# Kernel optimization log

Measured on AMD Instinct MI355X. Metric: run time of the kernel, lower is better.

The kernel has to match this reference:

```python
import jax, jax.numpy as jnp
import numpy as np

HIDDEN = 768
PDIM = int(HIDDEN / 4.67)  # 164
QK_DIM = 16
EPS = 1e-5


def setup_inputs() -> dict:
    key = jax.random.key(0)
    k_hs, k_qkv, k_out = jax.random.split(key, 3)
    B, S = 8, 2048
    hidden_states = jax.random.normal(k_hs, (B, S, HIDDEN), dtype=jnp.float32)
    qkv_out = 2 * QK_DIM + PDIM  # 196
    qkv_w = jax.random.normal(k_qkv, (qkv_out, PDIM), dtype=jnp.float32) * (PDIM ** -0.5)
    qkv_b = jnp.zeros((qkv_out,), dtype=jnp.float32)
    out_w = jax.random.normal(k_out, (HIDDEN, HIDDEN), dtype=jnp.float32) * (HIDDEN ** -0.5)
    out_b = jnp.zeros((HIDDEN,), dtype=jnp.float32)
    ln_scale = jnp.ones((PDIM,), dtype=jnp.float32)
    ln_bias = jnp.zeros((PDIM,), dtype=jnp.float32)
    return {
        "hidden_states": hidden_states,
        "ln_scale": ln_scale,
        "ln_bias": ln_bias,
        "qkv_w": qkv_w,
        "qkv_b": qkv_b,
        "out_w": out_w,
        "out_b": out_b,
    }


def reference(hidden_states, ln_scale, ln_bias, qkv_w, qkv_b, out_w, out_b):
    # channel split
    x1 = hidden_states[..., :PDIM]   # [B,S,pdim]
    x2 = hidden_states[..., PDIM:]   # [B,S,hidden-pdim]
    # LayerNorm over last dim
    mean = jnp.mean(x1, axis=-1, keepdims=True)
    var = jnp.mean(jnp.square(x1 - mean), axis=-1, keepdims=True)
    x1n = (x1 - mean) * jax.lax.rsqrt(var + EPS) * ln_scale + ln_bias
    # qkv projection: [B,S,2*qk+pdim]
    qkv = jnp.einsum("bsd,od->bso", x1n, qkv_w) + qkv_b
    q = qkv[..., :QK_DIM]
    k = qkv[..., QK_DIM:2 * QK_DIM]
    v = qkv[..., 2 * QK_DIM:]
    scale = QK_DIM ** -0.5
    scores = jnp.einsum("bqd,bkd->bqk", q, k) * scale  # [B,S,S]
    probs = jax.nn.softmax(scores, axis=-1)
    attended = jnp.einsum("bqk,bkd->bqd", probs, v)  # [B,S,pdim]
    merged = jnp.concatenate([attended, x2], axis=-1)  # [B,S,hidden]
    out = jnp.einsum("bsd,od->bso", merged, out_w) + out_b
    return out
```

## Files before the change

kernel.cpp:

```cpp
#include <hip/hip_runtime.h>
#include <hip/hip_bf16.h>

#define HID 768
#define PD 164
#define NQ 196
#define SEQ 2048

typedef __attribute__((ext_vector_type(8))) short bf16x8_t;
typedef __attribute__((ext_vector_type(4))) float f32x4_t;
typedef __attribute__((ext_vector_type(16))) float f32x16_t;
typedef __attribute__((ext_vector_type(4))) unsigned int u32x4_t;

static __device__ __forceinline__ unsigned short f2bfu(float f) {
  union { __hip_bfloat16 h; unsigned short u; } cv;
  cv.h = __float2bfloat16(f);
  return cv.u;
}

static __device__ __forceinline__ unsigned cvtpk(float a, float b) {
  unsigned r;
  asm("v_cvt_pk_bf16_f32 %0, %1, %2" : "=v"(r) : "v"(a), "v"(b));
  return r;
}

static __device__ __forceinline__ void gload16(const void* g, void* l) {
  __builtin_amdgcn_global_load_lds(
      (const __attribute__((address_space(1))) void*)g,
      (__attribute__((address_space(3))) void*)l, 16, 0, 0);
}

__global__ __launch_bounds__(256) void k_prep_q(const float* __restrict__ qkv_w,
                                                unsigned short* __restrict__ qwb) {
  int i = (blockIdx.x * 256 + threadIdx.x) * 4;
  if (i >= 39936) return;
  int n = i / 192, k = i - n * 192;
  float v0 = (n < NQ && k + 0 < PD) ? qkv_w[n * PD + k + 0] : 0.f;
  float v1 = (n < NQ && k + 1 < PD) ? qkv_w[n * PD + k + 1] : 0.f;
  float v2 = (n < NQ && k + 2 < PD) ? qkv_w[n * PD + k + 2] : 0.f;
  float v3 = (n < NQ && k + 3 < PD) ? qkv_w[n * PD + k + 3] : 0.f;
  ushort4 o;
  o.x = f2bfu(v0); o.y = f2bfu(v1); o.z = f2bfu(v2); o.w = f2bfu(v3);
  *(ushort4*)(qwb + i) = o;
}

__global__ __launch_bounds__(256, 2) void k_lnqkv(const float* __restrict__ hidden,
                                                  const float* __restrict__ lns,
                                                  const float* __restrict__ lnb,
                                                  const unsigned short* __restrict__ qwb,
                                                  const float* __restrict__ qkv_b,
                                                  const float* __restrict__ out_w,
                                                  unsigned short* __restrict__ wbo,
                                                  unsigned short* __restrict__ merged,
                                                  unsigned short* __restrict__ qg,
                                                  unsigned short* __restrict__ kg,
                                                  unsigned short* __restrict__ v16) {
  __shared__ float xr[64][172];
  __shared__ float stats[64][2];
  __shared__ unsigned short Aq[64][200];
  int t = threadIdx.x;
  if (blockIdx.x >= 256) {
    int i = ((blockIdx.x - 256) * 256 + t) * 4;
    float4 v = *(const float4*)(out_w + i);
    ushort4 o;
    o.x = f2bfu(v.x); o.y = f2bfu(v.y); o.z = f2bfu(v.z); o.w = f2bfu(v.w);
    *(ushort4*)(wbo + i) = o;
    return;
  }
  int r0 = blockIdx.x * 64;
  #pragma unroll
  for (int i = 0; i < 11; i++) {
    int idx = t + i * 256;
    if (idx < 2624) {
      int row = idx / 41, q = idx - row * 41;
      float4 v = *(const float4*)(hidden + (size_t)(r0 + row) * HID + q * 4);
      *(float4*)&xr[row][q * 4] = v;
    }
  }
  __syncthreads();
  {
    int l = t & 63, w = t >> 6;
    int row = w * 16 + (l & 15), g = l >> 4;
    float sum = 0.f, sq = 0.f;
    #pragma unroll
    for (int j = 0; j < 41; j++) {
      float x = xr[row][g * 41 + j];
      sum += x; sq += x * x;
    }
    sum += __shfl_xor(sum, 16, 64); sum += __shfl_xor(sum, 32, 64);
    sq  += __shfl_xor(sq, 16, 64);  sq  += __shfl_xor(sq, 32, 64);
    float mean = sum * (1.f / PD);
    float var = sq * (1.f / PD) - mean * mean;
    float rstd = rsqrtf(var + 1e-5f);
    if (g == 0) { stats[row][0] = mean; stats[row][1] = rstd; }
  }
  __syncthreads();
  #pragma unroll
  for (int i = 0; i < 24; i++) {
    int idx = t + i * 256;
    int row = idx / 96, c2 = idx - row * 96;
    int d = c2 * 2;
    float mean = stats[row][0], rstd = stats[row][1];
    float v0 = (d < PD)     ? (xr[row][d]     - mean) * rstd * lns[d]     + lnb[d]     : 0.f;
    float v1 = (d + 1 < PD) ? (xr[row][d + 1] - mean) * rstd * lns[d + 1] + lnb[d + 1] : 0.f;
    unsigned int pk = (unsigned int)f2bfu(v0) | ((unsigned int)f2bfu(v1) << 16);
    *(unsigned int*)(&Aq[row][d]) = pk;
  }
  #pragma unroll
  for (int i = 0; i < 38; i++) {
    int idx = t + i * 256;
    if (idx < 9664) {
      int row = idx / 151, q = idx - row * 151;
      int d = PD + q * 4;
      float4 v = *(const float4*)(hidden + (size_t)(r0 + row) * HID + d);
      ushort4 o;
      o.x = f2bfu(v.x); o.y = f2bfu(v.y); o.z = f2bfu(v.z); o.w = f2bfu(v.w);
      *(ushort4*)(merged + (size_t)(r0 + row) * HID + d) = o;
    }
  }
  __syncthreads();
  int l = t & 63, w = t >> 6, lr15 = l & 15, g = l >> 4;
  f32x4_t acc[13];
  #pragma unroll
  for (int n = 0; n < 13; n++) acc[n] = (f32x4_t){0.f, 0.f, 0.f, 0.f};
  #pragma unroll 2
  for (int kc = 0; kc < 6; kc++) {
    bf16x8_t a = *(const bf16x8_t*)(&Aq[w * 16 + lr15][kc * 32 + g * 8]);
    #pragma unroll
    for (int n = 0; n < 13; n++) {
      bf16x8_t b = *(const bf16x8_t*)(qwb + (size_t)(n * 16 + lr15) * 192 + kc * 32 + g * 8);
      acc[n] = __builtin_amdgcn_mfma_f32_16x16x32_bf16(a, b, acc[n], 0, 0, 0);
    }
  }
  {
    float bias = qkv_b[lr15];
    #pragma unroll
    for (int r = 0; r < 4; r++) {
      int grow = r0 + w * 16 + g * 4 + r;
      qg[(size_t)grow * 16 + lr15] = f2bfu((acc[0][r] + bias) * 0.36067376022224085f);
    }
  }
  {
    float bias = qkv_b[16 + lr15];
    #pragma unroll
    for (int r = 0; r < 4; r++) {
      int grow = r0 + w * 16 + g * 4 + r;
      kg[(size_t)grow * 16 + lr15] = f2bfu(acc[1][r] + bias);
    }
  }
  int s0 = (r0 & 2047) + w * 16;
  int bb = r0 >> 11;
  size_t vrowbase = (size_t)(bb * 128 + (s0 >> 4)) * 192;
  #pragma unroll
  for (int n = 2; n < 13; n++) {
    int col = n * 16 + lr15;
    int d = col - 32;
    float bias = (col < NQ) ? qkv_b[col] : 0.f;
    float v0 = acc[n][0] + bias, v1 = acc[n][1] + bias;
    float v2 = acc[n][2] + bias, v3 = acc[n][3] + bias;
    if (d == 164) { v0 = v1 = v2 = v3 = 1.f; }
    else if (d >= PD) { v0 = v1 = v2 = v3 = 0.f; }
    ushort4 o;
    o.x = f2bfu(v0); o.y = f2bfu(v1); o.z = f2bfu(v2); o.w = f2bfu(v3);
    *(ushort4*)(v16 + (vrowbase + d) * 16 + g * 4) = o;
  }
}

__global__ __launch_bounds__(256, 2) void k_attn(const unsigned short* __restrict__ qg,
                                                 const unsigned short* __restrict__ kg,
                                                 const unsigned short* __restrict__ v16,
                                                 unsigned short* __restrict__ merged) {
  __shared__ float red[2][64 * 98];
  int t = threadIdx.x;
  int w = t >> 6, l = t & 63;
  int b = blockIdx.x & 7, qt = blockIdx.x >> 3;
  int lo = l & 31, hi = l >> 5;
  int qbase = b * SEQ + qt * 32;
  bf16x8_t qf = *(const bf16x8_t*)(qg + (size_t)(qbase + lo) * 16 + hi * 8);
  const unsigned short* kb = kg + (size_t)b * SEQ * 16;
  const unsigned short* vbb = v16 + (size_t)b * 128 * 192 * 16;
  f32x16_t zro;
  #pragma unroll
  for (int r = 0; r < 16; r++) zro[r] = 0.f;
  f32x16_t acc[6];
  #pragma unroll
  for (int f = 0; f < 6; f++) acc[f] = zro;

  int it0 = w * 8;
  bf16x8_t kf0 = *(const bf16x8_t*)(kb + (size_t)(it0 * 64 + lo) * 16 + hi * 8);
  bf16x8_t kf1 = *(const bf16x8_t*)(kb + (size_t)(it0 * 64 + 32 + lo) * 16 + hi * 8);
  bf16x8_t va[6], vb_[6];
  {
    const unsigned short* vt0 = vbb + (size_t)(it0 * 4) * (192 * 16) + hi * 8;
    #pragma unroll
    for (int f = 0; f < 6; f++) va[f] = *(const bf16x8_t*)(vt0 + (f * 32 + lo) * 16);
  }
  for (int it = it0; it < it0 + 8; ++it) {
    bf16x8_t nk0 = *(const bf16x8_t*)(kb + (size_t)((it + 1) * 64 + lo) * 16 + hi * 8);
    bf16x8_t nk1 = *(const bf16x8_t*)(kb + (size_t)((it + 1) * 64 + 32 + lo) * 16 + hi * 8);
    f32x16_t sc0 = __builtin_amdgcn_mfma_f32_32x32x16_bf16(kf0, qf, zro, 0, 0, 0);
    f32x16_t sc1 = __builtin_amdgcn_mfma_f32_32x32x16_bf16(kf1, qf, zro, 0, 0, 0);
    bf16x8_t pa[4];
    #pragma unroll
    for (int jt = 0; jt < 2; ++jt) {
      f32x16_t sc = jt ? sc1 : sc0;
      unsigned u[8];
      #pragma unroll
      for (int k = 0; k < 8; ++k)
        u[k] = cvtpk(exp2f(sc[2 * k]), exp2f(sc[2 * k + 1]));
      asm volatile("v_permlane32_swap_b32 %0, %1" : "+v"(u[0]), "+v"(u[2]));
      asm volatile("v_permlane32_swap_b32 %0, %1" : "+v"(u[1]), "+v"(u[3]));
      asm volatile("v_permlane32_swap_b32 %0, %1" : "+v"(u[4]), "+v"(u[6]));
      asm volatile("v_permlane32_swap_b32 %0, %1" : "+v"(u[5]), "+v"(u[7]));
      union { u32x4_t u4; bf16x8_t h8; } c0, c1;
      c0.u4 = (u32x4_t){u[0], u[1], u[2], u[3]};
      c1.u4 = (u32x4_t){u[4], u[5], u[6], u[7]};
      pa[jt * 2 + 0] = c0.h8;
      pa[jt * 2 + 1] = c1.h8;
    }
#define PV_STEP(JS, VCUR, VNXT, NT, NJS)                                            \
    {                                                                               \
      const unsigned short* vtn = vbb + (size_t)((NT) * 4 + (NJS)) * (192 * 16) + hi * 8; \
      _Pragma("unroll")                                                             \
      for (int f = 0; f < 6; f++) VNXT[f] = *(const bf16x8_t*)(vtn + (f * 32 + lo) * 16); \
      _Pragma("unroll")                                                             \
      for (int f = 0; f < 6; f++)                                                   \
        acc[f] = __builtin_amdgcn_mfma_f32_32x32x16_bf16(pa[JS], VCUR[f], acc[f], 0, 0, 0); \
    }
    PV_STEP(0, va,  vb_, it, 1)
    PV_STEP(1, vb_, va,  it, 2)
    PV_STEP(2, va,  vb_, it, 3)
    PV_STEP(3, vb_, va,  it + 1, 0)
#undef PV_STEP
    kf0 = nk0; kf1 = nk1;
  }

  if (w >= 2) {
    float* dst = &red[w - 2][l * 98];
    #pragma unroll
    for (int f = 0; f < 6; f++)
      #pragma unroll
      for (int r = 0; r < 16; r += 2)
        *(float2*)(dst + f * 16 + r) = make_float2(acc[f][r], acc[f][r + 1]);
  }
  __syncthreads();
  if (w < 2) {
    const float* src = &red[w][l * 98];
    #pragma unroll
    for (int f = 0; f < 6; f++)
      #pragma unroll
      for (int r = 0; r < 16; r += 2) {
        float2 v = *(const float2*)(src + f * 16 + r);
        acc[f][r] += v.x; acc[f][r + 1] += v.y;
      }
  }
  __syncthreads();
  if (w == 1) {
    float* dst = &red[0][l * 98];
    #pragma unroll
    for (int f = 0; f < 6; f++)
      #pragma unroll
      for (int r = 0; r < 16; r += 2)
        *(float2*)(dst + f * 16 + r) = make_float2(acc[f][r], acc[f][r + 1]);
  }
  __syncthreads();
  if (w == 0) {
    const float* src = &red[0][l * 98];
    #pragma unroll
    for (int f = 0; f < 6; f++)
      #pragma unroll
      for (int r = 0; r < 16; r += 2) {
        float2 v = *(const float2*)(src + f * 16 + r);
        acc[f][r] += v.x; acc[f][r + 1] += v.y;
      }
    float dninv[16];
    #pragma unroll
    for (int r = 0; r < 16; ++r)
      dninv[r] = 1.0f / __shfl(acc[5][r], 4 + hi * 32, 64);
    #pragma unroll
    for (int f = 0; f < 6; ++f) {
      int d = f * 32 + lo;
      if (d < PD) {
        #pragma unroll
        for (int r = 0; r < 16; ++r) {
          int q = qbase + (r & 3) + 8 * (r >> 2) + 4 * hi;
          merged[(size_t)q * HID + d] = f2bfu(acc[f][r] * dninv[r]);
        }
      }
    }
  }
}

__global__ __launch_bounds__(256, 3) void k_out(const unsigned short* __restrict__ mg,
                                                const unsigned short* __restrict__ wb,
                                                const float* __restrict__ out_b,
                                                float* __restrict__ out) {
  __shared__ unsigned short Al[2][128 * 32];
  __shared__ unsigned short Bl[2][128 * 32];
  int t = threadIdx.x;
  int bid = blockIdx.x;
  int wgid = (bid & 7) * 96 + (bid >> 3);
  int nb = wgid % 6, mb = wgid / 6;
  int m0 = mb * 128, n0 = nb * 128;
  int l = t & 63, w = t >> 6, wr = w >> 1, wc = w & 1;
  int lr = l & 15, lg = l >> 4;
  int sw = (lr >> 1) & 3;
  f32x4_t acc[4][4];
  #pragma unroll
  for (int mi = 0; mi < 4; mi++)
    #pragma unroll
    for (int ni = 0; ni < 4; ni++) acc[mi][ni] = (f32x4_t){0.f, 0.f, 0.f, 0.f};

  auto stage = [&](int buf, int kt) {
    #pragma unroll
    for (int i = 0; i < 2; i++) {
      int off = t + i * 256;
      int row = off >> 2, c = off & 3;
      int cs = c ^ ((row >> 1) & 3);
      gload16(mg + (size_t)(m0 + row) * HID + kt * 32 + cs * 8, (char*)&Al[buf][0] + off * 16);
    }
    #pragma unroll
    for (int i = 0; i < 2; i++) {
      int off = t + i * 256;
      int row = off >> 2, c = off & 3;
      int cs = c ^ ((row >> 1) & 3);
      gload16(wb + (size_t)(n0 + row) * HID + kt * 32 + cs * 8, (char*)&Bl[buf][0] + off * 16);
    }
  };
  auto compute = [&](int cur) {
    __builtin_amdgcn_s_setprio(1);
    bf16x8_t a[4], bfr[4];
    int slot = lg ^ sw;
    #pragma unroll
    for (int mi = 0; mi < 4; mi++)
      a[mi] = *(const bf16x8_t*)(&Al[cur][(wr * 64 + mi * 16 + lr) * 32 + slot * 8]);
    #pragma unroll
    for (int ni = 0; ni < 4; ni++)
      bfr[ni] = *(const bf16x8_t*)(&Bl[cur][(wc * 64 + ni * 16 + lr) * 32 + slot * 8]);
    #pragma unroll
    for (int mi = 0; mi < 4; mi++)
      #pragma unroll
      for (int ni = 0; ni < 4; ni++)
        acc[mi][ni] = __builtin_amdgcn_mfma_f32_16x16x32_bf16(a[mi], bfr[ni], acc[mi][ni], 0, 0, 0);
    __builtin_amdgcn_s_setprio(0);
  };

  stage(0, 0);
  stage(1, 1);
  for (int kt = 0; kt < 23; kt++) {
    int cur = kt & 1;
    asm volatile("s_waitcnt vmcnt(4)" ::: "memory");
    __builtin_amdgcn_sched_barrier(0);
    __builtin_amdgcn_s_barrier();
    compute(cur);
    asm volatile("s_waitcnt lgkmcnt(0)" ::: "memory");
    __builtin_amdgcn_sched_barrier(0);
    __builtin_amdgcn_s_barrier();
    if (kt + 2 < 24) stage(cur, kt + 2);
  }
  asm volatile("s_waitcnt vmcnt(0)" ::: "memory");
  __builtin_amdgcn_sched_barrier(0);
  __builtin_amdgcn_s_barrier();
  compute(1);

  #pragma unroll
  for (int ni = 0; ni < 4; ni++) {
    int col = n0 + wc * 64 + ni * 16 + lr;
    float bias = out_b[col];
    #pragma unroll
    for (int mi = 0; mi < 4; mi++) {
      #pragma unroll
      for (int r = 0; r < 4; r++) {
        int row = m0 + wr * 64 + mi * 16 + lg * 4 + r;
        out[(size_t)row * HID + col] = acc[mi][ni][r] + bias;
      }
    }
  }
}

extern "C" void kernel_launch(void* const* d_in, const int* in_sizes, int n_in,
                              void* d_out, int out_size, void* d_ws, size_t ws_size,
                              hipStream_t stream) {
  const float* hidden = (const float*)d_in[0];
  const float* lns    = (const float*)d_in[1];
  const float* lnb    = (const float*)d_in[2];
  const float* qkv_w  = (const float*)d_in[3];
  const float* qkv_b  = (const float*)d_in[4];
  const float* out_w  = (const float*)d_in[5];
  const float* out_b  = (const float*)d_in[6];
  char* ws = (char*)d_ws;
  unsigned short* qg  = (unsigned short*)(ws + 0);
  unsigned short* kg  = (unsigned short*)(ws + 524288);
  unsigned short* v16 = (unsigned short*)(ws + 1048576);
  unsigned short* qwb = (unsigned short*)(ws + 13631488);
  unsigned short* wb  = (unsigned short*)(ws + 13711360);
  unsigned short* mg  = (unsigned short*)(ws + 14891008);
  hipLaunchKernelGGL(k_prep_q, dim3(39),  dim3(256), 0, stream, qkv_w, qwb);
  hipLaunchKernelGGL(k_lnqkv,  dim3(832), dim3(256), 0, stream, hidden, lns, lnb, qwb, qkv_b,
                     out_w, wb, mg, qg, kg, v16);
  hipLaunchKernelGGL(k_attn,   dim3(512), dim3(256), 0, stream, qg, kg, v16, mg);
  hipLaunchKernelGGL(k_out,    dim3(768), dim3(256), 0, stream, mg, wb, out_b, (float*)d_out);
}
```

Before: 96.77 us.

## Halve LN+QKV row tile to 32 and split N columns across waves

The LayerNorm+QKV kernel now processes 32 rows per block instead of 64, doubling the grid to 512 compute blocks plus the weight-conversion blocks, and raises the occupancy hint to 4 blocks per CU. Within the QKV MFMA stage, the four waves split as two row groups times two column halves (7 and 6 N-tiles), cutting accumulator registers per wave. The LN statistics loop is vectorised with float4 loads and an 8-lane reduction. The aim is more parallelism and occupancy for this memory-bound prologue, at the cost of reloading qwb B fragments across more blocks.

Result: faster. 93.80 us (-3.1%).

```diff
diff --git a/kernel.cpp b/kernel.cpp
--- a/kernel.cpp
+++ b/kernel.cpp
@@ -43,7 +43,7 @@
   *(ushort4*)(qwb + i) = o;
 }
 
-__global__ __launch_bounds__(256, 2) void k_lnqkv(const float* __restrict__ hidden,
+__global__ __launch_bounds__(256, 4) void k_lnqkv(const float* __restrict__ hidden,
                                                   const float* __restrict__ lns,
                                                   const float* __restrict__ lnb,
                                                   const unsigned short* __restrict__ qwb,
@@ -54,23 +54,24 @@
                                                   unsigned short* __restrict__ qg,
                                                   unsigned short* __restrict__ kg,
                                                   unsigned short* __restrict__ v16) {
-  __shared__ float xr[64][172];
-  __shared__ float stats[64][2];
-  __shared__ unsigned short Aq[64][200];
+  __shared__ float xr[32][172];
+  __shared__ float stats[32][2];
+  __shared__ unsigned short Aq[32][200];
   int t = threadIdx.x;
-  if (blockIdx.x >= 256) {
-    int i = ((blockIdx.x - 256) * 256 + t) * 4;
+  if (blockIdx.x >= 512) {
+    int i = ((blockIdx.x - 512) * 256 + t) * 4;
     float4 v = *(const float4*)(out_w + i);
     ushort4 o;
     o.x = f2bfu(v.x); o.y = f2bfu(v.y); o.z = f2bfu(v.z); o.w = f2bfu(v.w);
     *(ushort4*)(wbo + i) = o;
     return;
   }
-  int r0 = blockIdx.x * 64;
-  #pragma unroll
-  for (int i = 0; i < 11; i++) {
+  int r0 = blockIdx.x * 32;
+  int l = t & 63, w = t >> 6;
+  #pragma unroll
+  for (int i = 0; i < 6; i++) {
     int idx = t + i * 256;
-    if (idx < 2624) {
+    if (idx < 1312) {
       int row = idx / 41, q = idx - row * 41;
       float4 v = *(const float4*)(hidden + (size_t)(r0 + row) * HID + q * 4);
       *(float4*)&xr[row][q * 4] = v;
@@ -78,24 +79,23 @@
   }
   __syncthreads();
   {
-    int l = t & 63, w = t >> 6;
-    int row = w * 16 + (l & 15), g = l >> 4;
+    int row = w * 8 + (l & 7), g8 = l >> 3;
     float sum = 0.f, sq = 0.f;
-    #pragma unroll
-    for (int j = 0; j < 41; j++) {
-      float x = xr[row][g * 41 + j];
-      sum += x; sq += x * x;
-    }
-    sum += __shfl_xor(sum, 16, 64); sum += __shfl_xor(sum, 32, 64);
-    sq  += __shfl_xor(sq, 16, 64);  sq  += __shfl_xor(sq, 32, 64);
+    for (int j = g8; j < 41; j += 8) {
+      float4 v = *(const float4*)&xr[row][j * 4];
+      sum += v.x + v.y + v.z + v.w;
+      sq  += v.x * v.x + v.y * v.y + v.z * v.z + v.w * v.w;
+    }
+    sum += __shfl_xor(sum, 8, 64); sum += __shfl_xor(sum, 16, 64); sum += __shfl_xor(sum, 32, 64);
+    sq  += __shfl_xor(sq, 8, 64);  sq  += __shfl_xor(sq, 16, 64);  sq  += __shfl_xor(sq, 32, 64);
     float mean = sum * (1.f / PD);
     float var = sq * (1.f / PD) - mean * mean;
     float rstd = rsqrtf(var + 1e-5f);
-    if (g == 0) { stats[row][0] = mean; stats[row][1] = rstd; }
-  }
-  __syncthreads();
-  #pragma unroll
-  for (int i = 0; i < 24; i++) {
+    if (g8 == 0) { stats[row][0] = mean; stats[row][1] = rstd; }
+  }
+  __syncthreads();
+  #pragma unroll
+  for (int i = 0; i < 12; i++) {
     int idx = t + i * 256;
     int row = idx / 96, c2 = idx - row * 96;
     int d = c2 * 2;
@@ -106,9 +106,9 @@
     *(unsigned int*)(&Aq[row][d]) = pk;
   }
   #pragma unroll
-  for (int i = 0; i < 38; i++) {
+  for (int i = 0; i < 19; i++) {
     int idx = t + i * 256;
-    if (idx < 9664) {
+    if (idx < 4832) {
       int row = idx / 151, q = idx - row * 151;
       int d = PD + q * 4;
       float4 v = *(const float4*)(hidden + (size_t)(r0 + row) * HID + d);
@@ -118,50 +118,69 @@
     }
   }
   __syncthreads();
-  int l = t & 63, w = t >> 6, lr15 = l & 15, g = l >> 4;
-  f32x4_t acc[13];
-  #pragma unroll
-  for (int n = 0; n < 13; n++) acc[n] = (f32x4_t){0.f, 0.f, 0.f, 0.f};
+  int lr15 = l & 15, g = l >> 4;
+  int wr = w & 1, nh = w >> 1;
+  int nbase = nh ? 7 : 0;
+  int ncnt  = nh ? 6 : 7;
+  f32x4_t acc[7];
+  #pragma unroll
+  for (int n = 0; n < 7; n++) acc[n] = (f32x4_t){0.f, 0.f, 0.f, 0.f};
   #pragma unroll 2
   for (int kc = 0; kc < 6; kc++) {
-    bf16x8_t a = *(const bf16x8_t*)(&Aq[w * 16 + lr15][kc * 32 + g * 8]);
-    #pragma unroll
-    for (int n = 0; n < 13; n++) {
-      bf16x8_t b = *(const bf16x8_t*)(qwb + (size_t)(n * 16 + lr15) * 192 + kc * 32 + g * 8);
-      acc[n] = __builtin_amdgcn_mfma_f32_16x16x32_bf16(a, b, acc[n], 0, 0, 0);
-    }
-  }
-  {
-    float bias = qkv_b[lr15];
-    #pragma unroll
-    for (int r = 0; r < 4; r++) {
-      int grow = r0 + w * 16 + g * 4 + r;
-      qg[(size_t)grow * 16 + lr15] = f2bfu((acc[0][r] + bias) * 0.36067376022224085f);
-    }
-  }
-  {
-    float bias = qkv_b[16 + lr15];
-    #pragma unroll
-    for (int r = 0; r < 4; r++) {
-      int grow = r0 + w * 16 + g * 4 + r;
-      kg[(size_t)grow * 16 + lr15] = f2bfu(acc[1][r] + bias);
-    }
-  }
-  int s0 = (r0 & 2047) + w * 16;
+    bf16x8_t a = *(const bf16x8_t*)(&Aq[wr * 16 + lr15][kc * 32 + g * 8]);
+    #pragma unroll
+    for (int ni = 0; ni < 7; ni++) {
+      if (ni < ncnt) {
+        int n = nbase + ni;
+        bf16x8_t b = *(const bf16x8_t*)(qwb + (size_t)(n * 16 + lr15) * 192 + kc * 32 + g * 8);
+        acc[ni] = __builtin_amdgcn_mfma_f32_16x16x32_bf16(a, b, acc[ni], 0, 0, 0);
+      }
+    }
+  }
+  int s0 = (r0 & 2047) + wr * 16;
   int bb = r0 >> 11;
   size_t vrowbase = (size_t)(bb * 128 + (s0 >> 4)) * 192;
-  #pragma unroll
-  for (int n = 2; n < 13; n++) {
-    int col = n * 16 + lr15;
-    int d = col - 32;
-    float bias = (col < NQ) ? qkv_b[col] : 0.f;
-    float v0 = acc[n][0] + bias, v1 = acc[n][1] + bias;
-    float v2 = acc[n][2] + bias, v3 = acc[n][3] + bias;
-    if (d == 164) { v0 = v1 = v2 = v3 = 1.f; }
-    else if (d >= PD) { v0 = v1 = v2 = v3 = 0.f; }
-    ushort4 o;
-    o.x = f2bfu(v0); o.y = f2bfu(v1); o.z = f2bfu(v2); o.w = f2bfu(v3);
-    *(ushort4*)(v16 + (vrowbase + d) * 16 + g * 4) = o;
+  if (nh == 0) {
+    {
+      float bias = qkv_b[lr15];
+      #pragma unroll
+      for (int r = 0; r < 4; r++) {
+        int grow = r0 + wr * 16 + g * 4 + r;
+        qg[(size_t)grow * 16 + lr15] = f2bfu((acc[0][r] + bias) * 0.36067376022224085f);
+      }
+    }
+    {
+      float bias = qkv_b[16 + lr15];
+      #pragma unroll
+      for (int r = 0; r < 4; r++) {
+        int grow = r0 + wr * 16 + g * 4 + r;
+        kg[(size_t)grow * 16 + lr15] = f2bfu(acc[1][r] + bias);
+      }
+    }
+    #pragma unroll
+    for (int ni = 2; ni < 7; ni++) {
+      int col = ni * 16 + lr15;
+      int d = col - 32;
+      float bias = qkv_b[col];
+      ushort4 o;
+      o.x = f2bfu(acc[ni][0] + bias); o.y = f2bfu(acc[ni][1] + bias);
+      o.z = f2bfu(acc[ni][2] + bias); o.w = f2bfu(acc[ni][3] + bias);
+      *(ushort4*)(v16 + (vrowbase + d) * 16 + g * 4) = o;
+    }
+  } else {
+    #pragma unroll
+    for (int ni = 0; ni < 6; ni++) {
+      int col = (7 + ni) * 16 + lr15;
+      int d = col - 32;
+      float bias = (col < NQ) ? qkv_b[col] : 0.f;
+      float v0 = acc[ni][0] + bias, v1 = acc[ni][1] + bias;
+      float v2 = acc[ni][2] + bias, v3 = acc[ni][3] + bias;
+      if (d == 164) { v0 = v1 = v2 = v3 = 1.f; }
+      else if (d >= PD) { v0 = v1 = v2 = v3 = 0.f; }
+      ushort4 o;
+      o.x = f2bfu(v0); o.y = f2bfu(v1); o.z = f2bfu(v2); o.w = f2bfu(v3);
+      *(ushort4*)(v16 + (vrowbase + d) * 16 + g * 4) = o;
+    }
   }
 }
 
@@ -394,9 +413,9 @@
   unsigned short* qwb = (unsigned short*)(ws + 13631488);
   unsigned short* wb  = (unsigned short*)(ws + 13711360);
   unsigned short* mg  = (unsigned short*)(ws + 14891008);
-  hipLaunchKernelGGL(k_prep_q, dim3(39),  dim3(256), 0, stream, qkv_w, qwb);
-  hipLaunchKernelGGL(k_lnqkv,  dim3(832), dim3(256), 0, stream, hidden, lns, lnb, qwb, qkv_b,
+  hipLaunchKernelGGL(k_prep_q, dim3(39),   dim3(256), 0, stream, qkv_w, qwb);
+  hipLaunchKernelGGL(k_lnqkv,  dim3(1088), dim3(256), 0, stream, hidden, lns, lnb, qwb, qkv_b,
                      out_w, wb, mg, qg, kg, v16);
-  hipLaunchKernelGGL(k_attn,   dim3(512), dim3(256), 0, stream, qg, kg, v16, mg);
-  hipLaunchKernelGGL(k_out,    dim3(768), dim3(256), 0, stream, mg, wb, out_b, (float*)d_out);
-}
+  hipLaunchKernelGGL(k_attn,   dim3(512),  dim3(256), 0, stream, qg, kg, v16, mg);
+  hipLaunchKernelGGL(k_out,    dim3(768),  dim3(256), 0, stream, mg, wb, out_b, (float*)d_out);
+}
```
